# Performance work log

Hardware: AMD Instinct MI355X
Metric: run time of the kernel (lower is better)

## Reference

```python
import jax, jax.numpy as jnp
import numpy as np

N_NODE = 100000
N_EDGE = 1600000
D_NODE = 32
D_EDGE = 16
D_OUT = 32
D_IN = 2 * D_NODE + D_EDGE  # 80
D_HID = 2 * D_IN            # 160


def setup_inputs() -> dict:
    key = jax.random.key(0)
    ks = jax.random.split(key, 6)
    nodes = jax.random.normal(ks[0], (N_NODE, D_NODE), dtype=jnp.float32)
    edges = jax.random.normal(ks[1], (N_EDGE, D_EDGE), dtype=jnp.float32)
    senders = jax.random.randint(ks[2], (N_EDGE,), 0, N_NODE, dtype=jnp.int64 if jax.config.jax_enable_x64 else jnp.int32)
    receivers = jax.random.randint(ks[3], (N_EDGE,), 0, N_NODE, dtype=jnp.int64 if jax.config.jax_enable_x64 else jnp.int32)
    # Linear params (fan-in scaled like torch's default init scale)
    W1 = jax.random.normal(ks[4], (D_IN, D_HID), dtype=jnp.float32) / np.sqrt(D_IN)
    b1 = jnp.zeros((D_HID,), dtype=jnp.float32)
    W2 = jax.random.normal(ks[5], (D_HID, D_OUT), dtype=jnp.float32) / np.sqrt(D_HID)
    b2 = jnp.zeros((D_OUT,), dtype=jnp.float32)
    return {"nodes": nodes, "edges": edges, "senders": senders,
            "receivers": receivers, "W1": W1, "b1": b1, "W2": W2, "b2": b2}


def reference(nodes, edges, senders, receivers, W1, b1, W2, b2):
    # gather sender/receiver node features and concat with edge features: [E, 2*d_node+d_edge]
    feats = jnp.concatenate([nodes[senders], nodes[receivers], edges], axis=1)
    h = jax.nn.sigmoid(feats @ W1 + b1)   # [E, 2*d_in]
    new_edges = h @ W2 + b2               # [E, d_edge_out]
    return new_edges
```

## Files before the change

kernel.cpp:

```cpp
#include <hip/hip_runtime.h>

#define NEDGE  1600000
#define NPT    (NEDGE / 16)
#define GRID   5000
#define NIT    (NPT / GRID)
#define NNODE  100000
#define NB_OFF 32768
#define WS_BYTES (65536 + NNODE * 32 * 2)

typedef float f32x4  __attribute__((ext_vector_type(4)));
typedef short short8 __attribute__((ext_vector_type(8)));

static __device__ __forceinline__ ushort f2bf(float f) {
  uint u = __builtin_bit_cast(uint, f);
  return (ushort)((u + 0x7FFFu + ((u >> 16) & 1u)) >> 16);
}
static __device__ __forceinline__ uint cvt_pk(float lo, float hi) {
  uint r; asm("v_cvt_pk_bf16_f32 %0, %1, %2" : "=v"(r) : "v"(lo), "v"(hi)); return r;
}
static __device__ __forceinline__ float vexp2(float x) {
  float r; asm("v_exp_f32 %0, %1" : "=v"(r) : "v"(x)); return r;
}
static __device__ __forceinline__ float vrcp(float x) {
  float r; asm("v_rcp_f32 %0, %1" : "=v"(r) : "v"(x)); return r;
}
static __device__ __forceinline__ short8 pack8(float4 a, float4 b) {
  uint4 u;
  u.x = cvt_pk(a.x, a.y); u.y = cvt_pk(a.z, a.w);
  u.z = cvt_pk(b.x, b.y); u.w = cvt_pk(b.z, b.w);
  return __builtin_bit_cast(short8, u);
}

__global__ void prep_frags(const float* __restrict__ W1, const float* __restrict__ b1,
                           const float* __restrict__ W2, ushort* __restrict__ ws) {
  const int idx = blockIdx.x * 256 + threadIdx.x;
  if (idx >= 20480) return;
  const int frag = idx >> 9;
  const int lane = (idx >> 3) & 63;
  const int j    = idx & 7;
  const int g = lane >> 4, c = lane & 15;
  ushort v;
  if (frag < 30) {
    const int wh = frag / 15, rem = frag % 15, mt = rem / 3, kt = rem % 3;
    const int k   = kt * 32 + g * 8 + j;
    const int hid = 32 * mt + 8 * (c >> 2) + 4 * wh + (c & 3);
    const float s = -1.44269504088896f;
    const float val = (k < 80) ? W1[k * 160 + hid] * s
                               : (k == 80 ? b1[hid] * s : 0.0f);
    v = f2bf(val);
  } else {
    const int f2 = frag - 30, wh = f2 / 5, kt = f2 % 5;
    const int k = kt * 32 + g * 8 + j;
    v = f2bf(W2[k * 32 + 16 * wh + c]);
  }
  ws[idx] = v;
}

__global__ void prep_nodes(const float* __restrict__ nodes, ushort* __restrict__ nb) {
  const int idx = blockIdx.x * 256 + threadIdx.x;
  if (idx >= NNODE * 4) return;
  const float4 a = ((const float4*)nodes)[idx * 2];
  const float4 b = ((const float4*)nodes)[idx * 2 + 1];
  *(short8*)(nb + (size_t)idx * 8) = pack8(a, b);
}

template <bool USE_WS>
__global__ __launch_bounds__(128) void edge_mlp(
    const float* __restrict__ nodes, const float* __restrict__ edges,
    const int* __restrict__ senders, const int* __restrict__ receivers,
    const float* __restrict__ W1, const float* __restrict__ b1,
    const float* __restrict__ W2, const float* __restrict__ b2,
    float* __restrict__ out, const ushort* __restrict__ ws)
{
  __shared__ uint2 X[2][2][5][64];

  const int lane = threadIdx.x & 63;
  const int wh   = threadIdx.x >> 6;
  const int g    = lane >> 4;
  const int c    = lane & 15;
  const ushort* nb = USE_WS ? (ws + NB_OFF) : nullptr;

  short8 w1f[5][3];
  short8 w2f[5];
  if constexpr (USE_WS) {
#pragma unroll
    for (int mt = 0; mt < 5; ++mt)
#pragma unroll
      for (int kt = 0; kt < 3; ++kt)
        w1f[mt][kt] = *(const short8*)(ws + ((wh * 15 + mt * 3 + kt) * 64 + lane) * 8);
#pragma unroll
    for (int kt = 0; kt < 5; ++kt)
      w2f[kt] = *(const short8*)(ws + ((30 + wh * 5 + kt) * 64 + lane) * 8);
  } else {
    const float s = -1.44269504088896f;
    const int hidb = 8 * (c >> 2) + 4 * wh + (c & 3);
#pragma unroll
    for (int mt = 0; mt < 5; ++mt)
#pragma unroll
      for (int kt = 0; kt < 3; ++kt) {
        const int hid = 32 * mt + hidb;
        uint d[4];
#pragma unroll
        for (int dw = 0; dw < 4; ++dw) {
          const int k0 = kt * 32 + g * 8 + dw * 2, k1 = k0 + 1;
          const float f0 = (k0 < 80) ? W1[k0 * 160 + hid] * s : (k0 == 80 ? b1[hid] * s : 0.f);
          const float f1 = (k1 < 80) ? W1[k1 * 160 + hid] * s : (k1 == 80 ? b1[hid] * s : 0.f);
          d[dw] = (uint)f2bf(f0) | ((uint)f2bf(f1) << 16);
        }
        w1f[mt][kt] = __builtin_bit_cast(short8, make_uint4(d[0], d[1], d[2], d[3]));
      }
#pragma unroll
    for (int kt = 0; kt < 5; ++kt) {
      uint d[4];
#pragma unroll
      for (int dw = 0; dw < 4; ++dw) {
        const int k = kt * 32 + g * 8 + dw * 2;
        d[dw] = (uint)f2bf(W2[k * 32 + wh * 16 + c]) |
                ((uint)f2bf(W2[(k + 1) * 32 + wh * 16 + c]) << 16);
      }
      w2f[kt] = __builtin_bit_cast(short8, make_uint4(d[0], d[1], d[2], d[3]));
    }
  }
  const float4 b2v = *(const float4*)(b2 + wh * 16 + g * 4);
  const f32x4 b2c = (f32x4){b2v.x, b2v.y, b2v.z, b2v.w};
  const f32x4 z4  = (f32x4){0.f, 0.f, 0.f, 0.f};
  const uint  cE0 = (g == 2) ? 0x3F80u : 0u;

  int t = blockIdx.x;
  int e = t * 16 + c;
  short8 bfS_p, bfR_p;
  float4 sn0, sn1, rn0, rn1;
  float4 ee0, ee1;
  {
    const int si = senders[e], ri = receivers[e];
    if constexpr (USE_WS) {
      bfS_p = *(const short8*)(nb + (size_t)si * 32 + g * 8);
      bfR_p = *(const short8*)(nb + (size_t)ri * 32 + g * 8);
    } else {
      const float* sp = nodes + (size_t)si * 32 + g * 8;
      sn0 = *(const float4*)sp;  sn1 = *(const float4*)(sp + 4);
      const float* rp = nodes + (size_t)ri * 32 + g * 8;
      rn0 = *(const float4*)rp;  rn1 = *(const float4*)(rp + 4);
    }
    const float* ep = edges + (size_t)e * 16 + (g & 1) * 8;
    ee0 = *(const float4*)ep;  ee1 = *(const float4*)(ep + 4);
  }
  int e1 = (t + GRID) * 16 + c;
  int si1 = senders[e1], ri1 = receivers[e1];

  for (int i = 0; i < NIT; ++i) {
    const int buf = i & 1;

    uint4 ue;
    ue.x = (g < 2) ? cvt_pk(ee0.x, ee0.y) : cE0;
    ue.y = (g < 2) ? cvt_pk(ee0.z, ee0.w) : 0u;
    ue.z = (g < 2) ? cvt_pk(ee1.x, ee1.y) : 0u;
    ue.w = (g < 2) ? cvt_pk(ee1.z, ee1.w) : 0u;
    const short8 bfE = __builtin_bit_cast(short8, ue);
    short8 bfS, bfR;
    if constexpr (USE_WS) { bfS = bfS_p;            bfR = bfR_p; }
    else                  { bfS = pack8(sn0, sn1);  bfR = pack8(rn0, rn1); }

    f32x4 acc[5];
#pragma unroll
    for (int mt = 0; mt < 5; ++mt)
      acc[mt] = __builtin_amdgcn_mfma_f32_16x16x32_bf16(w1f[mt][0], bfS, z4, 0, 0, 0);
#pragma unroll
    for (int mt = 0; mt < 5; ++mt)
      acc[mt] = __builtin_amdgcn_mfma_f32_16x16x32_bf16(w1f[mt][1], bfR, acc[mt], 0, 0, 0);
#pragma unroll
    for (int mt = 0; mt < 5; ++mt)
      acc[mt] = __builtin_amdgcn_mfma_f32_16x16x32_bf16(w1f[mt][2], bfE, acc[mt], 0, 0, 0);

    {
      int tn = t + GRID; if (tn >= NPT) tn = t;
      const int en = tn * 16 + c;
      const float* epn = edges + (size_t)en * 16 + (g & 1) * 8;
      ee0 = *(const float4*)epn;  ee1 = *(const float4*)(epn + 4);
      if constexpr (USE_WS) {
        bfS_p = *(const short8*)(nb + (size_t)si1 * 32 + g * 8);
        bfR_p = *(const short8*)(nb + (size_t)ri1 * 32 + g * 8);
      } else {
        const float* spn = nodes + (size_t)si1 * 32 + g * 8;
        sn0 = *(const float4*)spn;  sn1 = *(const float4*)(spn + 4);
        const float* rpn = nodes + (size_t)ri1 * 32 + g * 8;
        rn0 = *(const float4*)rpn;  rn1 = *(const float4*)(rpn + 4);
      }
      int t2 = t + 2 * GRID; if (t2 >= NPT) t2 = tn;
      const int e2 = t2 * 16 + c;
      si1 = senders[e2];  ri1 = receivers[e2];
    }

    uint pkA[5], pkB[5];
#pragma unroll
    for (int mt = 0; mt < 5; ++mt) {
      const float h0 = vrcp(1.0f + vexp2(acc[mt][0]));
      const float h1 = vrcp(1.0f + vexp2(acc[mt][1]));
      const float h2 = vrcp(1.0f + vexp2(acc[mt][2]));
      const float h3 = vrcp(1.0f + vexp2(acc[mt][3]));
      pkA[mt] = cvt_pk(h0, h1);
      pkB[mt] = cvt_pk(h2, h3);
    }

#pragma unroll
    for (int kt = 0; kt < 5; ++kt) X[wh][buf][kt][lane] = make_uint2(pkA[kt], pkB[kt]);
    asm volatile("s_waitcnt lgkmcnt(0)\n\ts_barrier" ::: "memory");
    uint2 q[5];
#pragma unroll
    for (int kt = 0; kt < 5; ++kt) q[kt] = X[wh ^ 1][buf][kt][lane];

    f32x4 o;
    if (wh == 0) {
      o = __builtin_amdgcn_mfma_f32_16x16x32_bf16(w2f[0],
            __builtin_bit_cast(short8, make_uint4(pkA[0], pkB[0], q[0].x, q[0].y)), b2c, 0, 0, 0);
#pragma unroll
      for (int kt = 1; kt < 5; ++kt)
        o = __builtin_amdgcn_mfma_f32_16x16x32_bf16(w2f[kt],
              __builtin_bit_cast(short8, make_uint4(pkA[kt], pkB[kt], q[kt].x, q[kt].y)), o, 0, 0, 0);
    } else {
      o = __builtin_amdgcn_mfma_f32_16x16x32_bf16(w2f[0],
            __builtin_bit_cast(short8, make_uint4(q[0].x, q[0].y, pkA[0], pkB[0])), b2c, 0, 0, 0);
#pragma unroll
      for (int kt = 1; kt < 5; ++kt)
        o = __builtin_amdgcn_mfma_f32_16x16x32_bf16(w2f[kt],
              __builtin_bit_cast(short8, make_uint4(q[kt].x, q[kt].y, pkA[kt], pkB[kt])), o, 0, 0, 0);
    }

    float4 st; st.x = o[0]; st.y = o[1]; st.z = o[2]; st.w = o[3];
    *(float4*)(out + (size_t)e * 32 + wh * 16 + g * 4) = st;

    t += GRID;
    e = t * 16 + c;
  }
}

extern "C" void kernel_launch(void* const* d_in, const int* in_sizes, int n_in,
                              void* d_out, int out_size, void* d_ws, size_t ws_size,
                              hipStream_t stream) {
  const float* nodes     = (const float*)d_in[0];
  const float* edges     = (const float*)d_in[1];
  const int*   senders   = (const int*)d_in[2];
  const int*   receivers = (const int*)d_in[3];
  const float* W1        = (const float*)d_in[4];
  const float* b1        = (const float*)d_in[5];
  const float* W2        = (const float*)d_in[6];
  const float* b2        = (const float*)d_in[7];
  float* out = (float*)d_out;

  if (ws_size >= (size_t)WS_BYTES) {
    ushort* ws = (ushort*)d_ws;
    prep_frags<<<80, 256, 0, stream>>>(W1, b1, W2, ws);
    prep_nodes<<<(NNODE * 4 + 255) / 256, 256, 0, stream>>>(nodes, ws + NB_OFF);
    edge_mlp<true><<<GRID, 128, 0, stream>>>(nodes, edges, senders, receivers,
                                             W1, b1, W2, b2, out, ws);
  } else {
    edge_mlp<false><<<GRID, 128, 0, stream>>>(nodes, edges, senders, receivers,
                                              W1, b1, W2, b2, out, nullptr);
  }
}
```

Baseline: 162.7 us.

## Process two edge tiles per iteration with deeper prefetch and split MFMA chains

The fast path now handles two interleaved 16-edge tiles per loop iteration with separate register sets, prefetching node and edge data two tiles ahead and index data four tiles ahead. The grid is halved so each block runs more iterations. The second-layer MFMA accumulation is split into two independent chains that are summed at the end, which shortens the dependency chain. The aim is more memory-level parallelism to hide gather latency, at the cost of more registers and fewer resident blocks.

Result: slower. 167.0 us (+2.7%).

```diff
diff --git a/kernel.cpp b/kernel.cpp
--- a/kernel.cpp
+++ b/kernel.cpp
@@ -2,7 +2,7 @@
 
 #define NEDGE  1600000
 #define NPT    (NEDGE / 16)
-#define GRID   5000
+#define GRID   2500
 #define NIT    (NPT / GRID)
 #define NNODE  100000
 #define NB_OFF 32768
@@ -64,62 +64,187 @@
   *(short8*)(nb + (size_t)idx * 8) = pack8(a, b);
 }
 
-template <bool USE_WS>
-__global__ __launch_bounds__(128) void edge_mlp(
+#define TILE_BODY(nS, nR, eE0, eE1, siN, riN, tcur, BUF)                            \
+  {                                                                                 \
+    uint4 ue;                                                                       \
+    ue.x = (g < 2) ? cvt_pk(eE0.x, eE0.y) : cE0;                                    \
+    ue.y = (g < 2) ? cvt_pk(eE0.z, eE0.w) : 0u;                                     \
+    ue.z = (g < 2) ? cvt_pk(eE1.x, eE1.y) : 0u;                                     \
+    ue.w = (g < 2) ? cvt_pk(eE1.z, eE1.w) : 0u;                                     \
+    const short8 bfE = __builtin_bit_cast(short8, ue);                              \
+    f32x4 acc[5];                                                                   \
+    _Pragma("unroll")                                                               \
+    for (int mt = 0; mt < 5; ++mt)                                                  \
+      acc[mt] = __builtin_amdgcn_mfma_f32_16x16x32_bf16(w1f[mt][0], nS, z4, 0, 0, 0); \
+    _Pragma("unroll")                                                               \
+    for (int mt = 0; mt < 5; ++mt)                                                  \
+      acc[mt] = __builtin_amdgcn_mfma_f32_16x16x32_bf16(w1f[mt][1], nR, acc[mt], 0, 0, 0); \
+    _Pragma("unroll")                                                               \
+    for (int mt = 0; mt < 5; ++mt)                                                  \
+      acc[mt] = __builtin_amdgcn_mfma_f32_16x16x32_bf16(w1f[mt][2], bfE, acc[mt], 0, 0, 0); \
+                \
+    nS = *(const short8*)(nb + (size_t)siN * 32 + g * 8);                           \
+    nR = *(const short8*)(nb + (size_t)riN * 32 + g * 8);                           \
+    {                                                                               \
+      int tp = tcur + 2 * GRID; if (tp >= NPT) tp = tcur;                           \
+      const float* epp = edges + (size_t)(tp * 16 + c) * 16 + (g & 1) * 8;          \
+      eE0 = *(const float4*)epp;  eE1 = *(const float4*)(epp + 4);                  \
+      int tq = tcur + 4 * GRID; if (tq >= NPT) tq = tcur;                           \
+      const int eq = tq * 16 + c;                                                   \
+      siN = senders[eq];  riN = receivers[eq];                                      \
+    }                                                                               \
+                        \
+    uint pkA[5], pkB[5];                                                            \
+    _Pragma("unroll")                                                               \
+    for (int mt = 0; mt < 5; ++mt) {                                                \
+      const float h0 = vrcp(1.0f + vexp2(acc[mt][0]));                              \
+      const float h1 = vrcp(1.0f + vexp2(acc[mt][1]));                              \
+      const float h2 = vrcp(1.0f + vexp2(acc[mt][2]));                              \
+      const float h3 = vrcp(1.0f + vexp2(acc[mt][3]));                              \
+      pkA[mt] = cvt_pk(h0, h1);                                                     \
+      pkB[mt] = cvt_pk(h2, h3);                                                     \
+    }                                                                               \
+    _Pragma("unroll")                                                               \
+    for (int kt = 0; kt < 5; ++kt) X[wh][BUF][kt][lane] = make_uint2(pkA[kt], pkB[kt]); \
+    asm volatile("s_waitcnt lgkmcnt(0)\n\ts_barrier" ::: "memory");                 \
+    uint2 q[5];                                                                     \
+    _Pragma("unroll")                                                               \
+    for (int kt = 0; kt < 5; ++kt) q[kt] = X[wh ^ 1][BUF][kt][lane];                \
+    f32x4 oa, ob;                                                                   \
+    if (wh == 0) {                                                                  \
+      oa = __builtin_amdgcn_mfma_f32_16x16x32_bf16(w2f[0],                          \
+             __builtin_bit_cast(short8, make_uint4(pkA[0], pkB[0], q[0].x, q[0].y)), b2c, 0, 0, 0); \
+      ob = __builtin_amdgcn_mfma_f32_16x16x32_bf16(w2f[1],                          \
+             __builtin_bit_cast(short8, make_uint4(pkA[1], pkB[1], q[1].x, q[1].y)), z4, 0, 0, 0);  \
+      oa = __builtin_amdgcn_mfma_f32_16x16x32_bf16(w2f[2],                          \
+             __builtin_bit_cast(short8, make_uint4(pkA[2], pkB[2], q[2].x, q[2].y)), oa, 0, 0, 0);  \
+      ob = __builtin_amdgcn_mfma_f32_16x16x32_bf16(w2f[3],                          \
+             __builtin_bit_cast(short8, make_uint4(pkA[3], pkB[3], q[3].x, q[3].y)), ob, 0, 0, 0);  \
+      oa = __builtin_amdgcn_mfma_f32_16x16x32_bf16(w2f[4],                          \
+             __builtin_bit_cast(short8, make_uint4(pkA[4], pkB[4], q[4].x, q[4].y)), oa, 0, 0, 0);  \
+    } else {                                                                        \
+      oa = __builtin_amdgcn_mfma_f32_16x16x32_bf16(w2f[0],                          \
+             __builtin_bit_cast(short8, make_uint4(q[0].x, q[0].y, pkA[0], pkB[0])), b2c, 0, 0, 0); \
+      ob = __builtin_amdgcn_mfma_f32_16x16x32_bf16(w2f[1],                          \
+             __builtin_bit_cast(short8, make_uint4(q[1].x, q[1].y, pkA[1], pkB[1])), z4, 0, 0, 0);  \
+      oa = __builtin_amdgcn_mfma_f32_16x16x32_bf16(w2f[2],                          \
+             __builtin_bit_cast(short8, make_uint4(q[2].x, q[2].y, pkA[2], pkB[2])), oa, 0, 0, 0);  \
+      ob = __builtin_amdgcn_mfma_f32_16x16x32_bf16(w2f[3],                          \
+             __builtin_bit_cast(short8, make_uint4(q[3].x, q[3].y, pkA[3], pkB[3])), ob, 0, 0, 0);  \
+      oa = __builtin_amdgcn_mfma_f32_16x16x32_bf16(w2f[4],                          \
+             __builtin_bit_cast(short8, make_uint4(q[4].x, q[4].y, pkA[4], pkB[4])), oa, 0, 0, 0);  \
+    }                                                                               \
+    const f32x4 o = oa + ob;                                                        \
+    float4 st; st.x = o[0]; st.y = o[1]; st.z = o[2]; st.w = o[3];                  \
+    *(float4*)(out + (size_t)(tcur * 16 + c) * 32 + wh * 16 + g * 4) = st;          \
+  }
+
+__global__ __launch_bounds__(128) void edge_mlp_fast(
+    const float* __restrict__ edges,
+    const int* __restrict__ senders, const int* __restrict__ receivers,
+    const float* __restrict__ b2, float* __restrict__ out,
+    const ushort* __restrict__ ws)
+{
+  __shared__ uint2 X[2][2][5][64];
+
+  const int lane = threadIdx.x & 63;
+  const int wh   = threadIdx.x >> 6;
+  const int g    = lane >> 4;
+  const int c    = lane & 15;
+  const ushort* nb = ws + NB_OFF;
+
+  short8 w1f[5][3];
+  short8 w2f[5];
+#pragma unroll
+  for (int mt = 0; mt < 5; ++mt)
+#pragma unroll
+    for (int kt = 0; kt < 3; ++kt)
+      w1f[mt][kt] = *(const short8*)(ws + ((wh * 15 + mt * 3 + kt) * 64 + lane) * 8);
+#pragma unroll
+  for (int kt = 0; kt < 5; ++kt)
+    w2f[kt] = *(const short8*)(ws + ((30 + wh * 5 + kt) * 64 + lane) * 8);
+
+  const float4 b2v = *(const float4*)(b2 + wh * 16 + g * 4);
+  const f32x4 b2c = (f32x4){b2v.x, b2v.y, b2v.z, b2v.w};
+  const f32x4 z4  = (f32x4){0.f, 0.f, 0.f, 0.f};
+  const uint  cE0 = (g == 2) ? 0x3F80u : 0u;
+
+  int t = blockIdx.x;
+
+  short8 nSA, nRA, nSB, nRB;
+  float4 eA0, eA1, eB0, eB1;
+  {
+    const int ea = t * 16 + c;
+    const int eb = ea + GRID * 16;
+    const int sa = senders[ea], ra = receivers[ea];
+    const int sb = senders[eb], rb = receivers[eb];
+    nSA = *(const short8*)(nb + (size_t)sa * 32 + g * 8);
+    nRA = *(const short8*)(nb + (size_t)ra * 32 + g * 8);
+    nSB = *(const short8*)(nb + (size_t)sb * 32 + g * 8);
+    nRB = *(const short8*)(nb + (size_t)rb * 32 + g * 8);
+    const float* pa = edges + (size_t)ea * 16 + (g & 1) * 8;
+    eA0 = *(const float4*)pa;  eA1 = *(const float4*)(pa + 4);
+    const float* pb = edges + (size_t)eb * 16 + (g & 1) * 8;
+    eB0 = *(const float4*)pb;  eB1 = *(const float4*)(pb + 4);
+  }
+  int si2, ri2, si3, ri3;
+  {
+    const int e2 = (t + 2 * GRID) * 16 + c;
+    const int e3 = (t + 3 * GRID) * 16 + c;
+    si2 = senders[e2];  ri2 = receivers[e2];
+    si3 = senders[e3];  ri3 = receivers[e3];
+  }
+
+  for (int k = 0; k < NIT / 2; ++k) {
+    TILE_BODY(nSA, nRA, eA0, eA1, si2, ri2, t, 0)
+    const int tb = t + GRID;
+    TILE_BODY(nSB, nRB, eB0, eB1, si3, ri3, tb, 1)
+    t += 2 * GRID;
+  }
+}
+
+__global__ __launch_bounds__(128) void edge_mlp_ref(
     const float* __restrict__ nodes, const float* __restrict__ edges,
     const int* __restrict__ senders, const int* __restrict__ receivers,
     const float* __restrict__ W1, const float* __restrict__ b1,
     const float* __restrict__ W2, const float* __restrict__ b2,
-    float* __restrict__ out, const ushort* __restrict__ ws)
+    float* __restrict__ out)
 {
   __shared__ uint2 X[2][2][5][64];
-
   const int lane = threadIdx.x & 63;
   const int wh   = threadIdx.x >> 6;
   const int g    = lane >> 4;
   const int c    = lane & 15;
-  const ushort* nb = USE_WS ? (ws + NB_OFF) : nullptr;
 
   short8 w1f[5][3];
   short8 w2f[5];
-  if constexpr (USE_WS) {
-#pragma unroll
-    for (int mt = 0; mt < 5; ++mt)
-#pragma unroll
-      for (int kt = 0; kt < 3; ++kt)
-        w1f[mt][kt] = *(const short8*)(ws + ((wh * 15 + mt * 3 + kt) * 64 + lane) * 8);
-#pragma unroll
-    for (int kt = 0; kt < 5; ++kt)
-      w2f[kt] = *(const short8*)(ws + ((30 + wh * 5 + kt) * 64 + lane) * 8);
-  } else {
-    const float s = -1.44269504088896f;
-    const int hidb = 8 * (c >> 2) + 4 * wh + (c & 3);
-#pragma unroll
-    for (int mt = 0; mt < 5; ++mt)
-#pragma unroll
-      for (int kt = 0; kt < 3; ++kt) {
-        const int hid = 32 * mt + hidb;
-        uint d[4];
-#pragma unroll
-        for (int dw = 0; dw < 4; ++dw) {
-          const int k0 = kt * 32 + g * 8 + dw * 2, k1 = k0 + 1;
-          const float f0 = (k0 < 80) ? W1[k0 * 160 + hid] * s : (k0 == 80 ? b1[hid] * s : 0.f);
-          const float f1 = (k1 < 80) ? W1[k1 * 160 + hid] * s : (k1 == 80 ? b1[hid] * s : 0.f);
-          d[dw] = (uint)f2bf(f0) | ((uint)f2bf(f1) << 16);
-        }
-        w1f[mt][kt] = __builtin_bit_cast(short8, make_uint4(d[0], d[1], d[2], d[3]));
+  const float s = -1.44269504088896f;
+  const int hidb = 8 * (c >> 2) + 4 * wh + (c & 3);
+#pragma unroll
+  for (int mt = 0; mt < 5; ++mt)
+#pragma unroll
+    for (int kt = 0; kt < 3; ++kt) {
+      const int hid = 32 * mt + hidb;
+      uint d[4];
+#pragma unroll
+      for (int dw = 0; dw < 4; ++dw) {
+        const int k0 = kt * 32 + g * 8 + dw * 2, k1 = k0 + 1;
+        const float f0 = (k0 < 80) ? W1[k0 * 160 + hid] * s : (k0 == 80 ? b1[hid] * s : 0.f);
+        const float f1 = (k1 < 80) ? W1[k1 * 160 + hid] * s : (k1 == 80 ? b1[hid] * s : 0.f);
+        d[dw] = (uint)f2bf(f0) | ((uint)f2bf(f1) << 16);
       }
-#pragma unroll
-    for (int kt = 0; kt < 5; ++kt) {
-      uint d[4];
-#pragma unroll
-      for (int dw = 0; dw < 4; ++dw) {
-        const int k = kt * 32 + g * 8 + dw * 2;
-        d[dw] = (uint)f2bf(W2[k * 32 + wh * 16 + c]) |
-                ((uint)f2bf(W2[(k + 1) * 32 + wh * 16 + c]) << 16);
-      }
-      w2f[kt] = __builtin_bit_cast(short8, make_uint4(d[0], d[1], d[2], d[3]));
-    }
+      w1f[mt][kt] = __builtin_bit_cast(short8, make_uint4(d[0], d[1], d[2], d[3]));
+    }
+#pragma unroll
+  for (int kt = 0; kt < 5; ++kt) {
+    uint d[4];
+#pragma unroll
+    for (int dw = 0; dw < 4; ++dw) {
+      const int k = kt * 32 + g * 8 + dw * 2;
+      d[dw] = (uint)f2bf(W2[k * 32 + wh * 16 + c]) |
+              ((uint)f2bf(W2[(k + 1) * 32 + wh * 16 + c]) << 16);
+    }
+    w2f[kt] = __builtin_bit_cast(short8, make_uint4(d[0], d[1], d[2], d[3]));
   }
   const float4 b2v = *(const float4*)(b2 + wh * 16 + g * 4);
   const f32x4 b2c = (f32x4){b2v.x, b2v.y, b2v.z, b2v.w};
@@ -128,20 +253,13 @@
 
   int t = blockIdx.x;
   int e = t * 16 + c;
-  short8 bfS_p, bfR_p;
-  float4 sn0, sn1, rn0, rn1;
-  float4 ee0, ee1;
+  float4 sn0, sn1, rn0, rn1, ee0, ee1;
   {
     const int si = senders[e], ri = receivers[e];
-    if constexpr (USE_WS) {
-      bfS_p = *(const short8*)(nb + (size_t)si * 32 + g * 8);
-      bfR_p = *(const short8*)(nb + (size_t)ri * 32 + g * 8);
-    } else {
-      const float* sp = nodes + (size_t)si * 32 + g * 8;
-      sn0 = *(const float4*)sp;  sn1 = *(const float4*)(sp + 4);
-      const float* rp = nodes + (size_t)ri * 32 + g * 8;
-      rn0 = *(const float4*)rp;  rn1 = *(const float4*)(rp + 4);
-    }
+    const float* sp = nodes + (size_t)si * 32 + g * 8;
+    sn0 = *(const float4*)sp;  sn1 = *(const float4*)(sp + 4);
+    const float* rp = nodes + (size_t)ri * 32 + g * 8;
+    rn0 = *(const float4*)rp;  rn1 = *(const float4*)(rp + 4);
     const float* ep = edges + (size_t)e * 16 + (g & 1) * 8;
     ee0 = *(const float4*)ep;  ee1 = *(const float4*)(ep + 4);
   }
@@ -150,16 +268,14 @@
 
   for (int i = 0; i < NIT; ++i) {
     const int buf = i & 1;
-
     uint4 ue;
     ue.x = (g < 2) ? cvt_pk(ee0.x, ee0.y) : cE0;
     ue.y = (g < 2) ? cvt_pk(ee0.z, ee0.w) : 0u;
     ue.z = (g < 2) ? cvt_pk(ee1.x, ee1.y) : 0u;
     ue.w = (g < 2) ? cvt_pk(ee1.z, ee1.w) : 0u;
     const short8 bfE = __builtin_bit_cast(short8, ue);
-    short8 bfS, bfR;
-    if constexpr (USE_WS) { bfS = bfS_p;            bfR = bfR_p; }
-    else                  { bfS = pack8(sn0, sn1);  bfR = pack8(rn0, rn1); }
+    const short8 bfS = pack8(sn0, sn1);
+    const short8 bfR = pack8(rn0, rn1);
 
     f32x4 acc[5];
 #pragma unroll
@@ -177,15 +293,10 @@
       const int en = tn * 16 + c;
       const float* epn = edges + (size_t)en * 16 + (g & 1) * 8;
       ee0 = *(const float4*)epn;  ee1 = *(const float4*)(epn + 4);
-      if constexpr (USE_WS) {
-        bfS_p = *(const short8*)(nb + (size_t)si1 * 32 + g * 8);
-        bfR_p = *(const short8*)(nb + (size_t)ri1 * 32 + g * 8);
-      } else {
-        const float* spn = nodes + (size_t)si1 * 32 + g * 8;
-        sn0 = *(const float4*)spn;  sn1 = *(const float4*)(spn + 4);
-        const float* rpn = nodes + (size_t)ri1 * 32 + g * 8;
-        rn0 = *(const float4*)rpn;  rn1 = *(const float4*)(rpn + 4);
-      }
+      const float* spn = nodes + (size_t)si1 * 32 + g * 8;
+      sn0 = *(const float4*)spn;  sn1 = *(const float4*)(spn + 4);
+      const float* rpn = nodes + (size_t)ri1 * 32 + g * 8;
+      rn0 = *(const float4*)rpn;  rn1 = *(const float4*)(rpn + 4);
       int t2 = t + 2 * GRID; if (t2 >= NPT) t2 = tn;
       const int e2 = t2 * 16 + c;
       si1 = senders[e2];  ri1 = receivers[e2];
@@ -201,7 +312,6 @@
       pkA[mt] = cvt_pk(h0, h1);
       pkB[mt] = cvt_pk(h2, h3);
     }
-
 #pragma unroll
     for (int kt = 0; kt < 5; ++kt) X[wh][buf][kt][lane] = make_uint2(pkA[kt], pkB[kt]);
     asm volatile("s_waitcnt lgkmcnt(0)\n\ts_barrier" ::: "memory");
@@ -209,23 +319,31 @@
 #pragma unroll
     for (int kt = 0; kt < 5; ++kt) q[kt] = X[wh ^ 1][buf][kt][lane];
 
-    f32x4 o;
+    f32x4 oa, ob;
     if (wh == 0) {
-      o = __builtin_amdgcn_mfma_f32_16x16x32_bf16(w2f[0],
-            __builtin_bit_cast(short8, make_uint4(pkA[0], pkB[0], q[0].x, q[0].y)), b2c, 0, 0, 0);
-#pragma unroll
-      for (int kt = 1; kt < 5; ++kt)
-        o = __builtin_amdgcn_mfma_f32_16x16x32_bf16(w2f[kt],
-              __builtin_bit_cast(short8, make_uint4(pkA[kt], pkB[kt], q[kt].x, q[kt].y)), o, 0, 0, 0);
+      oa = __builtin_amdgcn_mfma_f32_16x16x32_bf16(w2f[0],
+             __builtin_bit_cast(short8, make_uint4(pkA[0], pkB[0], q[0].x, q[0].y)), b2c, 0, 0, 0);
+      ob = __builtin_amdgcn_mfma_f32_16x16x32_bf16(w2f[1],
+             __builtin_bit_cast(short8, make_uint4(pkA[1], pkB[1], q[1].x, q[1].y)), z4, 0, 0, 0);
+      oa = __builtin_amdgcn_mfma_f32_16x16x32_bf16(w2f[2],
+             __builtin_bit_cast(short8, make_uint4(pkA[2], pkB[2], q[2].x, q[2].y)), oa, 0, 0, 0);
+      ob = __builtin_amdgcn_mfma_f32_16x16x32_bf16(w2f[3],
+             __builtin_bit_cast(short8, make_uint4(pkA[3], pkB[3], q[3].x, q[3].y)), ob, 0, 0, 0);
+      oa = __builtin_amdgcn_mfma_f32_16x16x32_bf16(w2f[4],
+             __builtin_bit_cast(short8, make_uint4(pkA[4], pkB[4], q[4].x, q[4].y)), oa, 0, 0, 0);
     } else {
-      o = __builtin_amdgcn_mfma_f32_16x16x32_bf16(w2f[0],
-            __builtin_bit_cast(short8, make_uint4(q[0].x, q[0].y, pkA[0], pkB[0])), b2c, 0, 0, 0);
-#pragma unroll
-      for (int kt = 1; kt < 5; ++kt)
-        o = __builtin_amdgcn_mfma_f32_16x16x32_bf16(w2f[kt],
-              __builtin_bit_cast(short8, make_uint4(q[kt].x, q[kt].y, pkA[kt], pkB[kt])), o, 0, 0, 0);
-    }
-
+      oa = __builtin_amdgcn_mfma_f32_16x16x32_bf16(w2f[0],
+             __builtin_bit_cast(short8, make_uint4(q[0].x, q[0].y, pkA[0], pkB[0])), b2c, 0, 0, 0);
+      ob = __builtin_amdgcn_mfma_f32_16x16x32_bf16(w2f[1],
+             __builtin_bit_cast(short8, make_uint4(q[1].x, q[1].y, pkA[1], pkB[1])), z4, 0, 0, 0);
+      oa = __builtin_amdgcn_mfma_f32_16x16x32_bf16(w2f[2],
+             __builtin_bit_cast(short8, make_uint4(q[2].x, q[2].y, pkA[2], pkB[2])), oa, 0, 0, 0);
+      ob = __builtin_amdgcn_mfma_f32_16x16x32_bf16(w2f[3],
+             __builtin_bit_cast(short8, make_uint4(q[3].x, q[3].y, pkA[3], pkB[3])), ob, 0, 0, 0);
+      oa = __builtin_amdgcn_mfma_f32_16x16x32_bf16(w2f[4],
+             __builtin_bit_cast(short8, make_uint4(q[4].x, q[4].y, pkA[4], pkB[4])), oa, 0, 0, 0);
+    }
+    const f32x4 o = oa + ob;
     float4 st; st.x = o[0]; st.y = o[1]; st.z = o[2]; st.w = o[3];
     *(float4*)(out + (size_t)e * 32 + wh * 16 + g * 4) = st;
 
@@ -251,10 +369,9 @@
     ushort* ws = (ushort*)d_ws;
     prep_frags<<<80, 256, 0, stream>>>(W1, b1, W2, ws);
     prep_nodes<<<(NNODE * 4 + 255) / 256, 256, 0, stream>>>(nodes, ws + NB_OFF);
-    edge_mlp<true><<<GRID, 128, 0, stream>>>(nodes, edges, senders, receivers,
-                                             W1, b1, W2, b2, out, ws);
+    edge_mlp_fast<<<GRID, 128, 0, stream>>>(edges, senders, receivers, b2, out, ws);
   } else {
-    edge_mlp<false><<<GRID, 128, 0, stream>>>(nodes, edges, senders, receivers,
-                                              W1, b1, W2, b2, out, nullptr);
-  }
-}
+    edge_mlp_ref<<<GRID, 128, 0, stream>>>(nodes, edges, senders, receivers,
+                                           W1, b1, W2, b2, out);
+  }
+}
```

## Software-pipeline first-layer MFMA of next tile with sigmoid/second layer

Applied to the files above, without the earlier changes.

Splits the templated kernel into a fast workspace-based kernel and a reference fallback. The fast kernel software-pipelines the edge loop: it issues the first-layer MFMAs for the next tile before the barrier and second-layer MFMAs of the current tile, prefetches gathers two steps ahead, and splits the second-layer accumulation into two independent chains. The grid is halved, so each block runs twice as many iterations. The goal is to hide MFMA latency and barrier stalls, at the cost of more live registers and fewer blocks in flight.

Result: slower. 177.9 us (+9.4%).

```diff
diff --git a/kernel.cpp b/kernel.cpp
--- a/kernel.cpp
+++ b/kernel.cpp
@@ -2,8 +2,9 @@
 
 #define NEDGE  1600000
 #define NPT    (NEDGE / 16)
-#define GRID   5000
+#define GRID   2500
 #define NIT    (NPT / GRID)
+#define ESTEP  (GRID * 16)
 #define NNODE  100000
 #define NB_OFF 32768
 #define WS_BYTES (65536 + NNODE * 32 * 2)
@@ -64,13 +65,11 @@
   *(short8*)(nb + (size_t)idx * 8) = pack8(a, b);
 }
 
-template <bool USE_WS>
-__global__ __launch_bounds__(128) void edge_mlp(
-    const float* __restrict__ nodes, const float* __restrict__ edges,
+__global__ __launch_bounds__(128) void edge_mlp_fast(
+    const float* __restrict__ edges,
     const int* __restrict__ senders, const int* __restrict__ receivers,
-    const float* __restrict__ W1, const float* __restrict__ b1,
-    const float* __restrict__ W2, const float* __restrict__ b2,
-    float* __restrict__ out, const ushort* __restrict__ ws)
+    const float* __restrict__ b2, float* __restrict__ out,
+    const ushort* __restrict__ ws)
 {
   __shared__ uint2 X[2][2][5][64];
 
@@ -78,119 +77,65 @@
   const int wh   = threadIdx.x >> 6;
   const int g    = lane >> 4;
   const int c    = lane & 15;
-  const ushort* nb = USE_WS ? (ws + NB_OFF) : nullptr;
+  const ushort* nb = ws + NB_OFF;
 
   short8 w1f[5][3];
+#pragma unroll
+  for (int mt = 0; mt < 5; ++mt)
+#pragma unroll
+    for (int kt = 0; kt < 3; ++kt)
+      w1f[mt][kt] = *(const short8*)(ws + ((wh * 15 + mt * 3 + kt) * 64 + lane) * 8);
   short8 w2f[5];
-  if constexpr (USE_WS) {
-#pragma unroll
-    for (int mt = 0; mt < 5; ++mt)
-#pragma unroll
-      for (int kt = 0; kt < 3; ++kt)
-        w1f[mt][kt] = *(const short8*)(ws + ((wh * 15 + mt * 3 + kt) * 64 + lane) * 8);
-#pragma unroll
-    for (int kt = 0; kt < 5; ++kt)
-      w2f[kt] = *(const short8*)(ws + ((30 + wh * 5 + kt) * 64 + lane) * 8);
-  } else {
-    const float s = -1.44269504088896f;
-    const int hidb = 8 * (c >> 2) + 4 * wh + (c & 3);
-#pragma unroll
-    for (int mt = 0; mt < 5; ++mt)
-#pragma unroll
-      for (int kt = 0; kt < 3; ++kt) {
-        const int hid = 32 * mt + hidb;
-        uint d[4];
-#pragma unroll
-        for (int dw = 0; dw < 4; ++dw) {
-          const int k0 = kt * 32 + g * 8 + dw * 2, k1 = k0 + 1;
-          const float f0 = (k0 < 80) ? W1[k0 * 160 + hid] * s : (k0 == 80 ? b1[hid] * s : 0.f);
-          const float f1 = (k1 < 80) ? W1[k1 * 160 + hid] * s : (k1 == 80 ? b1[hid] * s : 0.f);
-          d[dw] = (uint)f2bf(f0) | ((uint)f2bf(f1) << 16);
-        }
-        w1f[mt][kt] = __builtin_bit_cast(short8, make_uint4(d[0], d[1], d[2], d[3]));
-      }
-#pragma unroll
-    for (int kt = 0; kt < 5; ++kt) {
-      uint d[4];
-#pragma unroll
-      for (int dw = 0; dw < 4; ++dw) {
-        const int k = kt * 32 + g * 8 + dw * 2;
-        d[dw] = (uint)f2bf(W2[k * 32 + wh * 16 + c]) |
-                ((uint)f2bf(W2[(k + 1) * 32 + wh * 16 + c]) << 16);
-      }
-      w2f[kt] = __builtin_bit_cast(short8, make_uint4(d[0], d[1], d[2], d[3]));
-    }
-  }
+#pragma unroll
+  for (int kt = 0; kt < 5; ++kt)
+    w2f[kt] = *(const short8*)(ws + ((30 + wh * 5 + kt) * 64 + lane) * 8);
+
   const float4 b2v = *(const float4*)(b2 + wh * 16 + g * 4);
   const f32x4 b2c = (f32x4){b2v.x, b2v.y, b2v.z, b2v.w};
   const f32x4 z4  = (f32x4){0.f, 0.f, 0.f, 0.f};
   const uint  cE0 = (g == 2) ? 0x3F80u : 0u;
 
-  int t = blockIdx.x;
-  int e = t * 16 + c;
-  short8 bfS_p, bfR_p;
-  float4 sn0, sn1, rn0, rn1;
+  int e = blockIdx.x * 16 + c;
+
+  short8 nS, nR;
   float4 ee0, ee1;
   {
     const int si = senders[e], ri = receivers[e];
-    if constexpr (USE_WS) {
-      bfS_p = *(const short8*)(nb + (size_t)si * 32 + g * 8);
-      bfR_p = *(const short8*)(nb + (size_t)ri * 32 + g * 8);
-    } else {
-      const float* sp = nodes + (size_t)si * 32 + g * 8;
-      sn0 = *(const float4*)sp;  sn1 = *(const float4*)(sp + 4);
-      const float* rp = nodes + (size_t)ri * 32 + g * 8;
-      rn0 = *(const float4*)rp;  rn1 = *(const float4*)(rp + 4);
-    }
+    nS = *(const short8*)(nb + (size_t)si * 32 + g * 8);
+    nR = *(const short8*)(nb + (size_t)ri * 32 + g * 8);
     const float* ep = edges + (size_t)e * 16 + (g & 1) * 8;
     ee0 = *(const float4*)ep;  ee1 = *(const float4*)(ep + 4);
   }
-  int e1 = (t + GRID) * 16 + c;
-  int si1 = senders[e1], ri1 = receivers[e1];
-
-  for (int i = 0; i < NIT; ++i) {
-    const int buf = i & 1;
-
+  int si1 = senders[e + ESTEP], ri1 = receivers[e + ESTEP];
+
+  f32x4 acc[5];
+  {
     uint4 ue;
     ue.x = (g < 2) ? cvt_pk(ee0.x, ee0.y) : cE0;
     ue.y = (g < 2) ? cvt_pk(ee0.z, ee0.w) : 0u;
     ue.z = (g < 2) ? cvt_pk(ee1.x, ee1.y) : 0u;
     ue.w = (g < 2) ? cvt_pk(ee1.z, ee1.w) : 0u;
     const short8 bfE = __builtin_bit_cast(short8, ue);
-    short8 bfS, bfR;
-    if constexpr (USE_WS) { bfS = bfS_p;            bfR = bfR_p; }
-    else                  { bfS = pack8(sn0, sn1);  bfR = pack8(rn0, rn1); }
-
-    f32x4 acc[5];
-#pragma unroll
-    for (int mt = 0; mt < 5; ++mt)
-      acc[mt] = __builtin_amdgcn_mfma_f32_16x16x32_bf16(w1f[mt][0], bfS, z4, 0, 0, 0);
-#pragma unroll
-    for (int mt = 0; mt < 5; ++mt)
-      acc[mt] = __builtin_amdgcn_mfma_f32_16x16x32_bf16(w1f[mt][1], bfR, acc[mt], 0, 0, 0);
+#pragma unroll
+    for (int mt = 0; mt < 5; ++mt)
+      acc[mt] = __builtin_amdgcn_mfma_f32_16x16x32_bf16(w1f[mt][0], nS, z4, 0, 0, 0);
+#pragma unroll
+    for (int mt = 0; mt < 5; ++mt)
+      acc[mt] = __builtin_amdgcn_mfma_f32_16x16x32_bf16(w1f[mt][1], nR, acc[mt], 0, 0, 0);
 #pragma unroll
     for (int mt = 0; mt < 5; ++mt)
       acc[mt] = __builtin_amdgcn_mfma_f32_16x16x32_bf16(w1f[mt][2], bfE, acc[mt], 0, 0, 0);
-
-    {
-      int tn = t + GRID; if (tn >= NPT) tn = t;
-      const int en = tn * 16 + c;
-      const float* epn = edges + (size_t)en * 16 + (g & 1) * 8;
-      ee0 = *(const float4*)epn;  ee1 = *(const float4*)(epn + 4);
-      if constexpr (USE_WS) {
-        bfS_p = *(const short8*)(nb + (size_t)si1 * 32 + g * 8);
-        bfR_p = *(const short8*)(nb + (size_t)ri1 * 32 + g * 8);
-      } else {
-        const float* spn = nodes + (size_t)si1 * 32 + g * 8;
-        sn0 = *(const float4*)spn;  sn1 = *(const float4*)(spn + 4);
-        const float* rpn = nodes + (size_t)ri1 * 32 + g * 8;
-        rn0 = *(const float4*)rpn;  rn1 = *(const float4*)(rpn + 4);
-      }
-      int t2 = t + 2 * GRID; if (t2 >= NPT) t2 = tn;
-      const int e2 = t2 * 16 + c;
-      si1 = senders[e2];  ri1 = receivers[e2];
-    }
-
+  }
+  {
+    nS = *(const short8*)(nb + (size_t)si1 * 32 + g * 8);
+    nR = *(const short8*)(nb + (size_t)ri1 * 32 + g * 8);
+    const float* ep = edges + (size_t)(e + ESTEP) * 16 + (g & 1) * 8;
+    ee0 = *(const float4*)ep;  ee1 = *(const float4*)(ep + 4);
+    si1 = senders[e + 2 * ESTEP];  ri1 = receivers[e + 2 * ESTEP];
+  }
+
+#pragma unroll 1
+  for (int i = 0; i < NIT - 1; ++i) {
     uint pkA[5], pkB[5];
 #pragma unroll
     for (int mt = 0; mt < 5; ++mt) {
@@ -201,31 +146,269 @@
       pkA[mt] = cvt_pk(h0, h1);
       pkB[mt] = cvt_pk(h2, h3);
     }
-
-#pragma unroll
-    for (int kt = 0; kt < 5; ++kt) X[wh][buf][kt][lane] = make_uint2(pkA[kt], pkB[kt]);
+#pragma unroll
+    for (int kt = 0; kt < 5; ++kt)
+      X[wh][i & 1][kt][lane] = make_uint2(pkA[kt], pkB[kt]);
+
+    f32x4 accN[5];
+    {
+      uint4 ue;
+      ue.x = (g < 2) ? cvt_pk(ee0.x, ee0.y) : cE0;
+      ue.y = (g < 2) ? cvt_pk(ee0.z, ee0.w) : 0u;
+      ue.z = (g < 2) ? cvt_pk(ee1.x, ee1.y) : 0u;
+      ue.w = (g < 2) ? cvt_pk(ee1.z, ee1.w) : 0u;
+      const short8 bfE = __builtin_bit_cast(short8, ue);
+#pragma unroll
+      for (int mt = 0; mt < 5; ++mt)
+        accN[mt] = __builtin_amdgcn_mfma_f32_16x16x32_bf16(w1f[mt][0], nS, z4, 0, 0, 0);
+#pragma unroll
+      for (int mt = 0; mt < 5; ++mt)
+        accN[mt] = __builtin_amdgcn_mfma_f32_16x16x32_bf16(w1f[mt][1], nR, accN[mt], 0, 0, 0);
+#pragma unroll
+      for (int mt = 0; mt < 5; ++mt)
+        accN[mt] = __builtin_amdgcn_mfma_f32_16x16x32_bf16(w1f[mt][2], bfE, accN[mt], 0, 0, 0);
+    }
+
+    {
+      nS = *(const short8*)(nb + (size_t)si1 * 32 + g * 8);
+      nR = *(const short8*)(nb + (size_t)ri1 * 32 + g * 8);
+      const int off2 = (i + 2 < NIT) ? 2 * ESTEP : 0;
+      const float* ep = edges + (size_t)(e + off2) * 16 + (g & 1) * 8;
+      ee0 = *(const float4*)ep;  ee1 = *(const float4*)(ep + 4);
+      const int off3 = (i + 3 < NIT) ? 3 * ESTEP : 0;
+      si1 = senders[e + off3];  ri1 = receivers[e + off3];
+    }
+
+    __builtin_amdgcn_sched_barrier(0);
+    asm volatile("s_waitcnt lgkmcnt(0)\n\ts_barrier" ::: "memory");
+
+    {
+      uint2 q[5];
+#pragma unroll
+      for (int kt = 0; kt < 5; ++kt) q[kt] = X[wh ^ 1][i & 1][kt][lane];
+      f32x4 oa, ob;
+      if (wh == 0) {
+        oa = __builtin_amdgcn_mfma_f32_16x16x32_bf16(w2f[0],
+               __builtin_bit_cast(short8, make_uint4(pkA[0], pkB[0], q[0].x, q[0].y)), b2c, 0, 0, 0);
+        ob = __builtin_amdgcn_mfma_f32_16x16x32_bf16(w2f[1],
+               __builtin_bit_cast(short8, make_uint4(pkA[1], pkB[1], q[1].x, q[1].y)), z4, 0, 0, 0);
+        oa = __builtin_amdgcn_mfma_f32_16x16x32_bf16(w2f[2],
+               __builtin_bit_cast(short8, make_uint4(pkA[2], pkB[2], q[2].x, q[2].y)), oa, 0, 0, 0);
+        ob = __builtin_amdgcn_mfma_f32_16x16x32_bf16(w2f[3],
+               __builtin_bit_cast(short8, make_uint4(pkA[3], pkB[3], q[3].x, q[3].y)), ob, 0, 0, 0);
+        oa = __builtin_amdgcn_mfma_f32_16x16x32_bf16(w2f[4],
+               __builtin_bit_cast(short8, make_uint4(pkA[4], pkB[4], q[4].x, q[4].y)), oa, 0, 0, 0);
+      } else {
+        oa = __builtin_amdgcn_mfma_f32_16x16x32_bf16(w2f[0],
+               __builtin_bit_cast(short8, make_uint4(q[0].x, q[0].y, pkA[0], pkB[0])), b2c, 0, 0, 0);
+        ob = __builtin_amdgcn_mfma_f32_16x16x32_bf16(w2f[1],
+               __builtin_bit_cast(short8, make_uint4(q[1].x, q[1].y, pkA[1], pkB[1])), z4, 0, 0, 0);
+        oa = __builtin_amdgcn_mfma_f32_16x16x32_bf16(w2f[2],
+               __builtin_bit_cast(short8, make_uint4(q[2].x, q[2].y, pkA[2], pkB[2])), oa, 0, 0, 0);
+        ob = __builtin_amdgcn_mfma_f32_16x16x32_bf16(w2f[3],
+               __builtin_bit_cast(short8, make_uint4(q[3].x, q[3].y, pkA[3], pkB[3])), ob, 0, 0, 0);
+        oa = __builtin_amdgcn_mfma_f32_16x16x32_bf16(w2f[4],
+               __builtin_bit_cast(short8, make_uint4(q[4].x, q[4].y, pkA[4], pkB[4])), oa, 0, 0, 0);
+      }
+      const f32x4 o = oa + ob;
+      float4 st; st.x = o[0]; st.y = o[1]; st.z = o[2]; st.w = o[3];
+      *(float4*)(out + (size_t)e * 32 + wh * 16 + g * 4) = st;
+    }
+
+#pragma unroll
+    for (int mt = 0; mt < 5; ++mt) acc[mt] = accN[mt];
+    e += ESTEP;
+  }
+
+  {
+    uint pkA[5], pkB[5];
+#pragma unroll
+    for (int mt = 0; mt < 5; ++mt) {
+      const float h0 = vrcp(1.0f + vexp2(acc[mt][0]));
+      const float h1 = vrcp(1.0f + vexp2(acc[mt][1]));
+      const float h2 = vrcp(1.0f + vexp2(acc[mt][2]));
+      const float h3 = vrcp(1.0f + vexp2(acc[mt][3]));
+      pkA[mt] = cvt_pk(h0, h1);
+      pkB[mt] = cvt_pk(h2, h3);
+    }
+#pragma unroll
+    for (int kt = 0; kt < 5; ++kt)
+      X[wh][1][kt][lane] = make_uint2(pkA[kt], pkB[kt]);
     asm volatile("s_waitcnt lgkmcnt(0)\n\ts_barrier" ::: "memory");
     uint2 q[5];
 #pragma unroll
-    for (int kt = 0; kt < 5; ++kt) q[kt] = X[wh ^ 1][buf][kt][lane];
-
-    f32x4 o;
+    for (int kt = 0; kt < 5; ++kt) q[kt] = X[wh ^ 1][1][kt][lane];
+    f32x4 oa, ob;
     if (wh == 0) {
-      o = __builtin_amdgcn_mfma_f32_16x16x32_bf16(w2f[0],
-            __builtin_bit_cast(short8, make_uint4(pkA[0], pkB[0], q[0].x, q[0].y)), b2c, 0, 0, 0);
-#pragma unroll
-      for (int kt = 1; kt < 5; ++kt)
-        o = __builtin_amdgcn_mfma_f32_16x16x32_bf16(w2f[kt],
-              __builtin_bit_cast(short8, make_uint4(pkA[kt], pkB[kt], q[kt].x, q[kt].y)), o, 0, 0, 0);
+      oa = __builtin_amdgcn_mfma_f32_16x16x32_bf16(w2f[0],
+             __builtin_bit_cast(short8, make_uint4(pkA[0], pkB[0], q[0].x, q[0].y)), b2c, 0, 0, 0);
+      ob = __builtin_amdgcn_mfma_f32_16x16x32_bf16(w2f[1],
+             __builtin_bit_cast(short8, make_uint4(pkA[1], pkB[1], q[1].x, q[1].y)), z4, 0, 0, 0);
+      oa = __builtin_amdgcn_mfma_f32_16x16x32_bf16(w2f[2],
+             __builtin_bit_cast(short8, make_uint4(pkA[2], pkB[2], q[2].x, q[2].y)), oa, 0, 0, 0);
+      ob = __builtin_amdgcn_mfma_f32_16x16x32_bf16(w2f[3],
+             __builtin_bit_cast(short8, make_uint4(pkA[3], pkB[3], q[3].x, q[3].y)), ob, 0, 0, 0);
+      oa = __builtin_amdgcn_mfma_f32_16x16x32_bf16(w2f[4],
+             __builtin_bit_cast(short8, make_uint4(pkA[4], pkB[4], q[4].x, q[4].y)), oa, 0, 0, 0);
     } else {
-      o = __builtin_amdgcn_mfma_f32_16x16x32_bf16(w2f[0],
-            __builtin_bit_cast(short8, make_uint4(q[0].x, q[0].y, pkA[0], pkB[0])), b2c, 0, 0, 0);
-#pragma unroll
-      for (int kt = 1; kt < 5; ++kt)
-        o = __builtin_amdgcn_mfma_f32_16x16x32_bf16(w2f[kt],
-              __builtin_bit_cast(short8, make_uint4(q[kt].x, q[kt].y, pkA[kt], pkB[kt])), o, 0, 0, 0);
-    }
-
+      oa = __builtin_amdgcn_mfma_f32_16x16x32_bf16(w2f[0],
+             __builtin_bit_cast(short8, make_uint4(q[0].x, q[0].y, pkA[0], pkB[0])), b2c, 0, 0, 0);
+      ob = __builtin_amdgcn_mfma_f32_16x16x32_bf16(w2f[1],
+             __builtin_bit_cast(short8, make_uint4(q[1].x, q[1].y, pkA[1], pkB[1])), z4, 0, 0, 0);
+      oa = __builtin_amdgcn_mfma_f32_16x16x32_bf16(w2f[2],
+             __builtin_bit_cast(short8, make_uint4(q[2].x, q[2].y, pkA[2], pkB[2])), oa, 0, 0, 0);
+      ob = __builtin_amdgcn_mfma_f32_16x16x32_bf16(w2f[3],
+             __builtin_bit_cast(short8, make_uint4(q[3].x, q[3].y, pkA[3], pkB[3])), ob, 0, 0, 0);
+      oa = __builtin_amdgcn_mfma_f32_16x16x32_bf16(w2f[4],
+             __builtin_bit_cast(short8, make_uint4(q[4].x, q[4].y, pkA[4], pkB[4])), oa, 0, 0, 0);
+    }
+    const f32x4 o = oa + ob;
+    float4 st; st.x = o[0]; st.y = o[1]; st.z = o[2]; st.w = o[3];
+    *(float4*)(out + (size_t)e * 32 + wh * 16 + g * 4) = st;
+  }
+}
+
+__global__ __launch_bounds__(128) void edge_mlp_ref(
+    const float* __restrict__ nodes, const float* __restrict__ edges,
+    const int* __restrict__ senders, const int* __restrict__ receivers,
+    const float* __restrict__ W1, const float* __restrict__ b1,
+    const float* __restrict__ W2, const float* __restrict__ b2,
+    float* __restrict__ out)
+{
+  __shared__ uint2 Xr[2][2][5][64];
+  const int lane = threadIdx.x & 63;
+  const int wh   = threadIdx.x >> 6;
+  const int g    = lane >> 4;
+  const int c    = lane & 15;
+
+  short8 w1f[5][3];
+  short8 w2f[5];
+  const float s = -1.44269504088896f;
+  const int hidb = 8 * (c >> 2) + 4 * wh + (c & 3);
+#pragma unroll
+  for (int mt = 0; mt < 5; ++mt)
+#pragma unroll
+    for (int kt = 0; kt < 3; ++kt) {
+      const int hid = 32 * mt + hidb;
+      uint d[4];
+#pragma unroll
+      for (int dw = 0; dw < 4; ++dw) {
+        const int k0 = kt * 32 + g * 8 + dw * 2, k1 = k0 + 1;
+        const float f0 = (k0 < 80) ? W1[k0 * 160 + hid] * s : (k0 == 80 ? b1[hid] * s : 0.f);
+        const float f1 = (k1 < 80) ? W1[k1 * 160 + hid] * s : (k1 == 80 ? b1[hid] * s : 0.f);
+        d[dw] = (uint)f2bf(f0) | ((uint)f2bf(f1) << 16);
+      }
+      w1f[mt][kt] = __builtin_bit_cast(short8, make_uint4(d[0], d[1], d[2], d[3]));
+    }
+#pragma unroll
+  for (int kt = 0; kt < 5; ++kt) {
+    uint d[4];
+#pragma unroll
+    for (int dw = 0; dw < 4; ++dw) {
+      const int k = kt * 32 + g * 8 + dw * 2;
+      d[dw] = (uint)f2bf(W2[k * 32 + wh * 16 + c]) |
+              ((uint)f2bf(W2[(k + 1) * 32 + wh * 16 + c]) << 16);
+    }
+    w2f[kt] = __builtin_bit_cast(short8, make_uint4(d[0], d[1], d[2], d[3]));
+  }
+  const float4 b2v = *(const float4*)(b2 + wh * 16 + g * 4);
+  const f32x4 b2c = (f32x4){b2v.x, b2v.y, b2v.z, b2v.w};
+  const f32x4 z4  = (f32x4){0.f, 0.f, 0.f, 0.f};
+  const uint  cE0 = (g == 2) ? 0x3F80u : 0u;
+
+  int t = blockIdx.x;
+  int e = t * 16 + c;
+  float4 sn0, sn1, rn0, rn1, ee0, ee1;
+  {
+    const int si = senders[e], ri = receivers[e];
+    const float* sp = nodes + (size_t)si * 32 + g * 8;
+    sn0 = *(const float4*)sp;  sn1 = *(const float4*)(sp + 4);
+    const float* rp = nodes + (size_t)ri * 32 + g * 8;
+    rn0 = *(const float4*)rp;  rn1 = *(const float4*)(rp + 4);
+    const float* ep = edges + (size_t)e * 16 + (g & 1) * 8;
+    ee0 = *(const float4*)ep;  ee1 = *(const float4*)(ep + 4);
+  }
+  int e1 = (t + GRID) * 16 + c;
+  int si1 = senders[e1], ri1 = receivers[e1];
+
+  for (int i = 0; i < NIT; ++i) {
+    const int buf = i & 1;
+    uint4 ue;
+    ue.x = (g < 2) ? cvt_pk(ee0.x, ee0.y) : cE0;
+    ue.y = (g < 2) ? cvt_pk(ee0.z, ee0.w) : 0u;
+    ue.z = (g < 2) ? cvt_pk(ee1.x, ee1.y) : 0u;
+    ue.w = (g < 2) ? cvt_pk(ee1.z, ee1.w) : 0u;
+    const short8 bfE = __builtin_bit_cast(short8, ue);
+    const short8 bfS = pack8(sn0, sn1);
+    const short8 bfR = pack8(rn0, rn1);
+
+    f32x4 acc[5];
+#pragma unroll
+    for (int mt = 0; mt < 5; ++mt)
+      acc[mt] = __builtin_amdgcn_mfma_f32_16x16x32_bf16(w1f[mt][0], bfS, z4, 0, 0, 0);
+#pragma unroll
+    for (int mt = 0; mt < 5; ++mt)
+      acc[mt] = __builtin_amdgcn_mfma_f32_16x16x32_bf16(w1f[mt][1], bfR, acc[mt], 0, 0, 0);
+#pragma unroll
+    for (int mt = 0; mt < 5; ++mt)
+      acc[mt] = __builtin_amdgcn_mfma_f32_16x16x32_bf16(w1f[mt][2], bfE, acc[mt], 0, 0, 0);
+
+    {
+      int tn = t + GRID; if (tn >= NPT) tn = t;
+      const int en = tn * 16 + c;
+      const float* epn = edges + (size_t)en * 16 + (g & 1) * 8;
+      ee0 = *(const float4*)epn;  ee1 = *(const float4*)(epn + 4);
+      const float* spn = nodes + (size_t)si1 * 32 + g * 8;
+      sn0 = *(const float4*)spn;  sn1 = *(const float4*)(spn + 4);
+      const float* rpn = nodes + (size_t)ri1 * 32 + g * 8;
+      rn0 = *(const float4*)rpn;  rn1 = *(const float4*)(rpn + 4);
+      int t2 = t + 2 * GRID; if (t2 >= NPT) t2 = tn;
+      const int e2 = t2 * 16 + c;
+      si1 = senders[e2];  ri1 = receivers[e2];
+    }
+
+    uint pkA[5], pkB[5];
+#pragma unroll
+    for (int mt = 0; mt < 5; ++mt) {
+      const float h0 = vrcp(1.0f + vexp2(acc[mt][0]));
+      const float h1 = vrcp(1.0f + vexp2(acc[mt][1]));
+      const float h2 = vrcp(1.0f + vexp2(acc[mt][2]));
+      const float h3 = vrcp(1.0f + vexp2(acc[mt][3]));
+      pkA[mt] = cvt_pk(h0, h1);
+      pkB[mt] = cvt_pk(h2, h3);
+    }
+#pragma unroll
+    for (int kt = 0; kt < 5; ++kt) Xr[wh][buf][kt][lane] = make_uint2(pkA[kt], pkB[kt]);
+    asm volatile("s_waitcnt lgkmcnt(0)\n\ts_barrier" ::: "memory");
+    uint2 q[5];
+#pragma unroll
+    for (int kt = 0; kt < 5; ++kt) q[kt] = Xr[wh ^ 1][buf][kt][lane];
+
+    f32x4 oa, ob;
+    if (wh == 0) {
+      oa = __builtin_amdgcn_mfma_f32_16x16x32_bf16(w2f[0],
+             __builtin_bit_cast(short8, make_uint4(pkA[0], pkB[0], q[0].x, q[0].y)), b2c, 0, 0, 0);
+      ob = __builtin_amdgcn_mfma_f32_16x16x32_bf16(w2f[1],
+             __builtin_bit_cast(short8, make_uint4(pkA[1], pkB[1], q[1].x, q[1].y)), z4, 0, 0, 0);
+      oa = __builtin_amdgcn_mfma_f32_16x16x32_bf16(w2f[2],
+             __builtin_bit_cast(short8, make_uint4(pkA[2], pkB[2], q[2].x, q[2].y)), oa, 0, 0, 0);
+      ob = __builtin_amdgcn_mfma_f32_16x16x32_bf16(w2f[3],
+             __builtin_bit_cast(short8, make_uint4(pkA[3], pkB[3], q[3].x, q[3].y)), ob, 0, 0, 0);
+      oa = __builtin_amdgcn_mfma_f32_16x16x32_bf16(w2f[4],
+             __builtin_bit_cast(short8, make_uint4(pkA[4], pkB[4], q[4].x, q[4].y)), oa, 0, 0, 0);
+    } else {
+      oa = __builtin_amdgcn_mfma_f32_16x16x32_bf16(w2f[0],
+             __builtin_bit_cast(short8, make_uint4(q[0].x, q[0].y, pkA[0], pkB[0])), b2c, 0, 0, 0);
+      ob = __builtin_amdgcn_mfma_f32_16x16x32_bf16(w2f[1],
+             __builtin_bit_cast(short8, make_uint4(q[1].x, q[1].y, pkA[1], pkB[1])), z4, 0, 0, 0);
+      oa = __builtin_amdgcn_mfma_f32_16x16x32_bf16(w2f[2],
+             __builtin_bit_cast(short8, make_uint4(q[2].x, q[2].y, pkA[2], pkB[2])), oa, 0, 0, 0);
+      ob = __builtin_amdgcn_mfma_f32_16x16x32_bf16(w2f[3],
+             __builtin_bit_cast(short8, make_uint4(q[3].x, q[3].y, pkA[3], pkB[3])), ob, 0, 0, 0);
+      oa = __builtin_amdgcn_mfma_f32_16x16x32_bf16(w2f[4],
+             __builtin_bit_cast(short8, make_uint4(q[4].x, q[4].y, pkA[4], pkB[4])), oa, 0, 0, 0);
+    }
+    const f32x4 o = oa + ob;
     float4 st; st.x = o[0]; st.y = o[1]; st.z = o[2]; st.w = o[3];
     *(float4*)(out + (size_t)e * 32 + wh * 16 + g * 4) = st;
 
@@ -251,10 +434,9 @@
     ushort* ws = (ushort*)d_ws;
     prep_frags<<<80, 256, 0, stream>>>(W1, b1, W2, ws);
     prep_nodes<<<(NNODE * 4 + 255) / 256, 256, 0, stream>>>(nodes, ws + NB_OFF);
-    edge_mlp<true><<<GRID, 128, 0, stream>>>(nodes, edges, senders, receivers,
-                                             W1, b1, W2, b2, out, ws);
+    edge_mlp_fast<<<GRID, 128, 0, stream>>>(edges, senders, receivers, b2, out, ws);
   } else {
-    edge_mlp<false><<<GRID, 128, 0, stream>>>(nodes, edges, senders, receivers,
-                                              W1, b1, W2, b2, out, nullptr);
-  }
-}
+    edge_mlp_ref<<<GRID, 128, 0, stream>>>(nodes, edges, senders, receivers,
+                                           W1, b1, W2, b2, out);
+  }
+}
```
